# Optimization experiments

Hardware: AMD Instinct MI355X
Metric: run time of the kernel (lower is better)

## Reference

```python
import jax, jax.numpy as jnp
import numpy as np

NEG = -9e15  # sentinel used by the torch module for masked logits


def setup_inputs() -> dict:
    key = jax.random.key(0)
    k_x, k_nl, k_q, k_k, k_v = jax.random.split(key, 5)
    n, m, nhid = 50000, 16, 128
    x = jax.random.normal(k_x, (n, nhid), dtype=jnp.float32)
    neighbor_list = jax.random.randint(k_nl, (n, m), 0, n)  # value n-1 == padding
    # xavier_uniform with gain=1.414 for square (nhid, nhid) matrices
    bound = 1.414 * np.sqrt(6.0 / (nhid + nhid))
    Q = jax.random.uniform(k_q, (nhid, nhid), jnp.float32, -bound, bound)
    K = jax.random.uniform(k_k, (nhid, nhid), jnp.float32, -bound, bound)
    V = jax.random.uniform(k_v, (nhid, nhid), jnp.float32, -bound, bound)
    return {"x": x, "neighbor_list": neighbor_list, "Q": Q, "K": K, "V": V}


def _forward(x, neighbor_list, Q, K, V):
    n, nhid = x.shape
    scare = jnp.asarray(nhid ** 0.5, x.dtype)
    # masks: neighbor index n-1 means padding
    mask = (neighbor_list != n - 1).astype(x.dtype)            # (n, m)
    mask1 = mask[:, :, None] * mask[:, None, :]                # (n, m, m)
    mask2 = jnp.concatenate([jnp.ones((n, 1), x.dtype), mask], axis=1)[:, None, :]  # (n,1,m+1)

    # ---- stage 1: neighbor-level attention ----
    nm = x[neighbor_list]                                      # (n, m, h) gather
    Qn = jnp.einsum('nmk,kh->nmh', nm, Q)
    Kn = jnp.einsum('nmk,kh->nmh', nm, K)
    Vn = jnp.einsum('nmk,kh->nmh', nm, V)
    s = jnp.einsum('nih,njh->nij', Qn, Kn)                     # (n, m, m)
    s = jax.nn.leaky_relu(s, 0.01)
    s = jnp.where(mask1 > 0, s, NEG) * scare                   # faithful: scale after mask
    a = jax.nn.softmax(s, axis=2)                              # dropout is identity (eval)
    nres = jnp.einsum('nij,njh->nih', a, Vn)                   # (n, m, h)

    # ---- stage 2: node-level attention over [self, neighbors] ----
    xr = x[:, None, :]                                         # (n, 1, h)
    cat = jnp.concatenate([xr, nres], axis=1)                  # (n, m+1, h)
    Qx = jnp.einsum('nik,kh->nih', xr, Q)                      # (n, 1, h)
    Kc = jnp.einsum('njk,kh->njh', cat, K)
    Vc = jnp.einsum('njk,kh->njh', cat, V)
    s2 = jnp.einsum('nih,njh->nij', Qx, Kc) * scare            # (n, 1, m+1)
    s2 = jax.nn.leaky_relu(s2, 0.01)
    s2 = jnp.where(mask2 > 0, s2, NEG)
    a2 = jax.nn.softmax(s2, axis=2)
    out = jnp.einsum('nij,njh->nih', a2, Vc)[:, 0, :]          # (n, h)

    # F.normalize: L2 along dim 1, eps 1e-12
    norm = jnp.linalg.norm(out, axis=1, keepdims=True)
    return out / jnp.maximum(norm, 1e-12)


def reference(x, neighbor_list, Q, K, V):
    return _forward(x, neighbor_list, Q, K, V)
```

## Files before the change

### kernel.cpp

```cpp
#include <hip/hip_runtime.h>
#include <math.h>

#define NEG_CONST (-9000000000000000.0f)
#define SCARE 11.313708498984761f

#define DPP_XOR1  0xB1
#define DPP_XOR2  0x4E
#define DPP_XOR7  0x141
#define DPP_XOR15 0x140

template<int CTRL>
__device__ __forceinline__ float dpp_add(float x) {
    int yi = __builtin_amdgcn_update_dpp(0, __float_as_int(x), CTRL, 0xF, 0xF, true);
    return x + __int_as_float(yi);
}
template<int CTRL>
__device__ __forceinline__ float dpp_max(float x) {
    int yi = __builtin_amdgcn_update_dpp(0, __float_as_int(x), CTRL, 0xF, 0xF, true);
    return fmaxf(x, __int_as_float(yi));
}

__device__ __forceinline__ void wave_lds_fence() {
    __builtin_amdgcn_wave_barrier();
    asm volatile("s_waitcnt lgkmcnt(0)" ::: "memory");
    __builtin_amdgcn_wave_barrier();
}

__global__ __launch_bounds__(256) void small_mm_a(const float* __restrict__ Q,
                                                  const float* __restrict__ K,
                                                  const float* __restrict__ V,
                                                  float* __restrict__ QKt,
                                                  float* __restrict__ VV) {
    int r  = blockIdx.x * 8 + (threadIdx.x >> 5);
    int c0 = (threadIdx.x & 31) * 4;
    float a0 = 0.f, a1 = 0.f, a2 = 0.f, a3 = 0.f;
    if (blockIdx.y == 0) {
        for (int k = 0; k < 128; k += 4) {
            float4 q  = *reinterpret_cast<const float4*>(&Q[r * 128 + k]);
            float4 k0 = *reinterpret_cast<const float4*>(&K[(c0 + 0) * 128 + k]);
            float4 k1 = *reinterpret_cast<const float4*>(&K[(c0 + 1) * 128 + k]);
            float4 k2 = *reinterpret_cast<const float4*>(&K[(c0 + 2) * 128 + k]);
            float4 k3 = *reinterpret_cast<const float4*>(&K[(c0 + 3) * 128 + k]);
            a0 += q.x*k0.x + q.y*k0.y + q.z*k0.z + q.w*k0.w;
            a1 += q.x*k1.x + q.y*k1.y + q.z*k1.z + q.w*k1.w;
            a2 += q.x*k2.x + q.y*k2.y + q.z*k2.z + q.w*k2.w;
            a3 += q.x*k3.x + q.y*k3.y + q.z*k3.z + q.w*k3.w;
        }
        float4 o = {a0, a1, a2, a3};
        *reinterpret_cast<float4*>(&QKt[r * 128 + c0]) = o;
    } else {
        for (int k = 0; k < 128; ++k) {
            float a = V[r * 128 + k];
            float4 b = *reinterpret_cast<const float4*>(&V[k * 128 + c0]);
            a0 += a * b.x; a1 += a * b.y; a2 += a * b.z; a3 += a * b.w;
        }
        float4 o = {a0, a1, a2, a3};
        *reinterpret_cast<float4*>(&VV[r * 128 + c0]) = o;
    }
}

__global__ __launch_bounds__(256) void small_mm_b(const float* __restrict__ QKt,
                                                  const float* __restrict__ V,
                                                  float* __restrict__ MT) {
    int r  = blockIdx.x * 8 + (threadIdx.x >> 5);
    int c0 = (threadIdx.x & 31) * 4;
    float a0 = 0.f, a1 = 0.f, a2 = 0.f, a3 = 0.f;
    for (int k = 0; k < 128; k += 4) {
        float4 q  = *reinterpret_cast<const float4*>(&QKt[r * 128 + k]);
        float4 k0 = *reinterpret_cast<const float4*>(&V[(c0 + 0) * 128 + k]);
        float4 k1 = *reinterpret_cast<const float4*>(&V[(c0 + 1) * 128 + k]);
        float4 k2 = *reinterpret_cast<const float4*>(&V[(c0 + 2) * 128 + k]);
        float4 k3 = *reinterpret_cast<const float4*>(&V[(c0 + 3) * 128 + k]);
        a0 += q.x*k0.x + q.y*k0.y + q.z*k0.z + q.w*k0.w;
        a1 += q.x*k1.x + q.y*k1.y + q.z*k1.z + q.w*k1.w;
        a2 += q.x*k2.x + q.y*k2.y + q.z*k2.z + q.w*k2.w;
        a3 += q.x*k3.x + q.y*k3.y + q.z*k3.z + q.w*k3.w;
    }
    float4 o = {a0, a1, a2, a3};
    *reinterpret_cast<float4*>(&MT[r * 128 + c0]) = o;
}

__global__ __launch_bounds__(256) void proj_gemm(
    const float* __restrict__ x,
    const float* __restrict__ W0, const float* __restrict__ W1,
    const float* __restrict__ W2, const float* __restrict__ W3,
    float* __restrict__ O0, float* __restrict__ O1,
    float* __restrict__ O2, float* __restrict__ O3, int n)
{
    __shared__ __align__(16) float xs[32][132];
    __shared__ __align__(16) float ws[32][132];

    const float* Wsel[4] = {W0, W1, W2, W3};
    float*       Osel[4] = {O0, O1, O2, O3};
    const float* W = Wsel[blockIdx.y];
    float*       O = Osel[blockIdx.y];
    int row0 = blockIdx.x * 128;
    int tid = threadIdx.x;
    int tr = tid >> 4, tc = tid & 15;

    float acc[8][8] = {};
    for (int kk = 0; kk < 128; kk += 32) {
        #pragma unroll
        for (int it = 0; it < 4; ++it) {
            int id = tid + it * 256;
            int r = id >> 3;
            int f = id & 7;
            int grow = row0 + r;
            float4 v = (grow < n)
                ? *reinterpret_cast<const float4*>(&x[(size_t)grow * 128 + kk + f * 4])
                : make_float4(0.f, 0.f, 0.f, 0.f);
            xs[f * 4 + 0][r] = v.x; xs[f * 4 + 1][r] = v.y;
            xs[f * 4 + 2][r] = v.z; xs[f * 4 + 3][r] = v.w;
        }
        #pragma unroll
        for (int it = 0; it < 4; ++it) {
            int id = tid + it * 256;
            int k = id >> 5;
            int c4 = id & 31;
            *reinterpret_cast<float4*>(&ws[k][c4 * 4]) =
                *reinterpret_cast<const float4*>(&W[(size_t)(kk + k) * 128 + c4 * 4]);
        }
        __syncthreads();
        #pragma unroll 4
        for (int k = 0; k < 32; ++k) {
            float4 a0 = *reinterpret_cast<const float4*>(&xs[k][tr * 8]);
            float4 a1 = *reinterpret_cast<const float4*>(&xs[k][tr * 8 + 4]);
            float4 b0 = *reinterpret_cast<const float4*>(&ws[k][tc * 8]);
            float4 b1 = *reinterpret_cast<const float4*>(&ws[k][tc * 8 + 4]);
            float av[8] = {a0.x, a0.y, a0.z, a0.w, a1.x, a1.y, a1.z, a1.w};
            float bv[8] = {b0.x, b0.y, b0.z, b0.w, b1.x, b1.y, b1.z, b1.w};
            #pragma unroll
            for (int i2 = 0; i2 < 8; ++i2)
                #pragma unroll
                for (int j2 = 0; j2 < 8; ++j2)
                    acc[i2][j2] += av[i2] * bv[j2];
        }
        __syncthreads();
    }
    #pragma unroll
    for (int i2 = 0; i2 < 8; ++i2) {
        int grow = row0 + tr * 8 + i2;
        if (grow < n) {
            float4 o0 = {acc[i2][0], acc[i2][1], acc[i2][2], acc[i2][3]};
            float4 o1 = {acc[i2][4], acc[i2][5], acc[i2][6], acc[i2][7]};
            *reinterpret_cast<float4*>(&O[(size_t)grow * 128 + tc * 8])     = o0;
            *reinterpret_cast<float4*>(&O[(size_t)grow * 128 + tc * 8 + 4]) = o1;
        }
    }
}

__global__ __launch_bounds__(256, 4) void node_attn(
    const int* __restrict__ nlist,
    const float* __restrict__ x,
    const float* __restrict__ xQK,
    const float* __restrict__ u,
    const float* __restrict__ xV,
    const float* __restrict__ xVV,
    float* __restrict__ outp, int n)
{
    __shared__ __align__(16) float Bs[4][16][132];
    __shared__ __align__(16) int   NLs[4][16];
    __shared__ __align__(16) float Ts[4][16];

    int tid = threadIdx.x;
    int wid = tid >> 6;
    int l   = tid & 63;
    int g   = l >> 2;
    int jj  = l & 3;
    int i = blockIdx.x * 4 + wid;
    if (i >= n) return;

    int nlv = 0;
    if (l < 16) {
        nlv = nlist[(size_t)i * 16 + l];
        NLs[wid][l] = nlv;
    }
    unsigned long long mb = __ballot(l < 16 ? (nlv != n - 1) : 0);
    int nl_g = __shfl(nlv, g, 64);

    float4 A[8];
    size_t rowbase = (size_t)nl_g * 128 + jj * 32;
    #pragma unroll
    for (int k4 = 0; k4 < 8; ++k4) {
        int rc = ((k4 + jj * 2) & 7) * 4;
        A[k4] = *reinterpret_cast<const float4*>(&xQK[rowbase + rc]);
    }
    #pragma unroll
    for (int k4 = 0; k4 < 8; ++k4) {
        int rc = ((k4 + jj * 2) & 7) * 4;
        float4 v = *reinterpret_cast<const float4*>(&x[rowbase + rc]);
        *reinterpret_cast<float4*>(&Bs[wid][g][jj * 32 + rc]) = v;
    }

    float2 qa = *reinterpret_cast<const float2*>(&xQK[(size_t)i * 128 + l * 2]);
    float2 xa = *reinterpret_cast<const float2*>(&x[(size_t)i * 128 + l * 2]);
    float s200 = qa.x * xa.x + qa.y * xa.y;
    s200 = dpp_add<DPP_XOR1>(s200);
    s200 = dpp_add<DPP_XOR2>(s200);
    s200 = dpp_add<DPP_XOR7>(s200);
    s200 = dpp_add<DPP_XOR15>(s200);
    s200 += __shfl_xor(s200, 16, 64);
    s200 += __shfl_xor(s200, 32, 64);

    wave_lds_fence();

    float a[16];
    {
        float sc[16];
        #pragma unroll
        for (int c = 0; c < 16; ++c) {
            float acc = 0.f;
            #pragma unroll
            for (int k4 = 0; k4 < 8; ++k4) {
                int rc = ((k4 + jj * 2) & 7) * 4;
                float4 b = *reinterpret_cast<const float4*>(&Bs[wid][c][jj * 32 + rc]);
                acc += A[k4].x * b.x + A[k4].y * b.y + A[k4].z * b.z + A[k4].w * b.w;
            }
            acc = dpp_add<DPP_XOR1>(acc);
            acc = dpp_add<DPP_XOR2>(acc);
            sc[c] = acc;
        }
        bool rlive = (mb >> g) & 1ULL;
        float m = -3.0e38f;
        #pragma unroll
        for (int c = 0; c < 16; ++c) {
            float s = sc[c];
            float slr = s > 0.f ? s : 0.01f * s;
            bool live = rlive && ((mb >> c) & 1ULL);
            float sm = (live ? slr : NEG_CONST) * SCARE;
            sc[c] = sm;
            m = fmaxf(m, sm);
        }
        float ssum = 0.f;
        #pragma unroll
        for (int c = 0; c < 16; ++c) { float p = __expf(sc[c] - m); a[c] = p; ssum += p; }
        float rs = 1.f / ssum;
        #pragma unroll
        for (int c = 0; c < 16; ++c) a[c] *= rs;
    }

    int nlarr[16];
    {
        int4 nlq[4];
        #pragma unroll
        for (int q4 = 0; q4 < 4; ++q4)
            nlq[q4] = *reinterpret_cast<const int4*>(&NLs[wid][q4 * 4]);
        #pragma unroll
        for (int q4 = 0; q4 < 4; ++q4) {
            nlarr[q4 * 4 + 0] = nlq[q4].x; nlarr[q4 * 4 + 1] = nlq[q4].y;
            nlarr[q4 * 4 + 2] = nlq[q4].z; nlarr[q4 * 4 + 3] = nlq[q4].w;
        }
    }
    float2 vvreg[16];
    #pragma unroll
    for (int k = 0; k < 16; ++k)
        vvreg[k] = *reinterpret_cast<const float2*>(&xVV[(size_t)nlarr[k] * 128 + l * 2]);

    {
        float acc = 0.f;
        #pragma unroll
        for (int k4 = 0; k4 < 8; ++k4) {
            int rc = ((k4 + jj * 2) & 7) * 4;
            float4 uu = *reinterpret_cast<const float4*>(&u[(size_t)i * 128 + jj * 32 + rc]);
            float4 b  = *reinterpret_cast<const float4*>(&Bs[wid][g][jj * 32 + rc]);
            acc += uu.x * b.x + uu.y * b.y + uu.z * b.z + uu.w * b.w;
        }
        acc = dpp_add<DPP_XOR1>(acc);
        acc = dpp_add<DPP_XOR2>(acc);
        if (jj == 0) Ts[wid][g] = acc;
    }
    wave_lds_fence();
    float tarr[16];
    {
        #pragma unroll
        for (int q4 = 0; q4 < 4; ++q4) {
            float4 t4 = *reinterpret_cast<const float4*>(&Ts[wid][q4 * 4]);
            tarr[q4 * 4 + 0] = t4.x; tarr[q4 * 4 + 1] = t4.y;
            tarr[q4 * 4 + 2] = t4.z; tarr[q4 * 4 + 3] = t4.w;
        }
    }

    float lg = 0.f;
    #pragma unroll
    for (int k = 0; k < 16; ++k) lg += a[k] * tarr[k];
    {
        float v = lg * SCARE;
        v = v > 0.f ? v : 0.01f * v;
        lg = ((mb >> g) & 1ULL) ? v : NEG_CONST;
    }
    float v0 = s200 * SCARE;
    v0 = v0 > 0.f ? v0 : 0.01f * v0;

    float m17 = lg;
    m17 = dpp_max<DPP_XOR7>(m17);
    m17 = dpp_max<DPP_XOR15>(m17);
    m17 = fmaxf(m17, __shfl_xor(m17, 16, 64));
    m17 = fmaxf(m17, __shfl_xor(m17, 32, 64));
    m17 = fmaxf(m17, v0);
    float pg = __expf(lg - m17);
    float sg = pg;
    sg = dpp_add<DPP_XOR7>(sg);
    sg = dpp_add<DPP_XOR15>(sg);
    sg += __shfl_xor(sg, 16, 64);
    sg += __shfl_xor(sg, 32, 64);
    float p0 = __expf(v0 - m17);
    float inv = 1.f / (sg + p0);
    float a2g = pg * inv;
    float a20 = p0 * inv;

    float w[16];
    #pragma unroll
    for (int k = 0; k < 16; ++k) {
        float wv = a2g * a[k];
        wv = dpp_add<DPP_XOR7>(wv);
        wv = dpp_add<DPP_XOR15>(wv);
        wv += __shfl_xor(wv, 16, 64);
        wv += __shfl_xor(wv, 32, 64);
        w[k] = wv;
    }

    float2 xv = *reinterpret_cast<const float2*>(&xV[(size_t)i * 128 + l * 2]);
    float o0 = a20 * xv.x, o1 = a20 * xv.y;
    #pragma unroll
    for (int k = 0; k < 16; ++k) {
        o0 += w[k] * vvreg[k].x;
        o1 += w[k] * vvreg[k].y;
    }
    float sq = o0 * o0 + o1 * o1;
    sq = dpp_add<DPP_XOR1>(sq);
    sq = dpp_add<DPP_XOR2>(sq);
    sq = dpp_add<DPP_XOR7>(sq);
    sq = dpp_add<DPP_XOR15>(sq);
    sq += __shfl_xor(sq, 16, 64);
    sq += __shfl_xor(sq, 32, 64);
    float d = fmaxf(sqrtf(sq), 1e-12f);
    float rd = 1.f / d;
    float2 o = {o0 * rd, o1 * rd};
    *reinterpret_cast<float2*>(&outp[(size_t)i * 128 + l * 2]) = o;
}

extern "C" void kernel_launch(void* const* d_in, const int* in_sizes, int n_in,
                              void* d_out, int out_size, void* d_ws, size_t ws_size,
                              hipStream_t stream) {
    const float* x     = (const float*)d_in[0];
    const int*   nlist = (const int*)d_in[1];
    const float* Q     = (const float*)d_in[2];
    const float* K     = (const float*)d_in[3];
    const float* V     = (const float*)d_in[4];
    float* out = (float*)d_out;
    int n = in_sizes[0] / 128;

    float* ws   = (float*)d_ws;
    float* QKt  = ws;
    float* MT   = ws + 16384;
    float* VV   = ws + 32768;
    float* xQK  = ws + 49152;
    size_t stride = (size_t)n * 128;
    float* uarr = xQK + stride;
    float* xV   = uarr + stride;
    float* xVV  = xV + stride;

    small_mm_a<<<dim3(16, 2), 256, 0, stream>>>(Q, K, V, QKt, VV);
    small_mm_b<<<dim3(16), 256, 0, stream>>>(QKt, V, MT);
    dim3 g2((n + 127) / 128, 4);
    proj_gemm<<<g2, 256, 0, stream>>>(x, QKt, MT, V, VV, xQK, uarr, xV, xVV, n);
    node_attn<<<(n + 3) / 4, 256, 0, stream>>>(nlist, x, xQK, uarr, xV, xVV, out, n);
}
```

Baseline: 316.4 us.

## Use direct global-to-LDS loads for neighbor rows with one wave per node

The node_attn kernel now runs one 64-thread wave per node instead of four waves per block. The gathered neighbor x rows go straight to LDS through global_load_lds, with a permuted layout so the score loop reads are conflict-free. This is meant to remove the register round trip for the staging copy and to let the xQK loads overlap with the async LDS fill. In exchange there are many more small blocks, and the code depends on the exact byte layout the LDS-direct loads produce.

```diff
diff --git a/kernel.cpp b/kernel.cpp
--- a/kernel.cpp
+++ b/kernel.cpp
@@ -23,6 +23,11 @@
 __device__ __forceinline__ void wave_lds_fence() {
     __builtin_amdgcn_wave_barrier();
     asm volatile("s_waitcnt lgkmcnt(0)" ::: "memory");
+    __builtin_amdgcn_wave_barrier();
+}
+__device__ __forceinline__ void wave_vm_fence() {
+    __builtin_amdgcn_wave_barrier();
+    asm volatile("s_waitcnt vmcnt(0) lgkmcnt(0)" ::: "memory");
     __builtin_amdgcn_wave_barrier();
 }
 
@@ -149,7 +154,7 @@
     }
 }
 
-__global__ __launch_bounds__(256, 4) void node_attn(
+__global__ __launch_bounds__(64, 5) void node_attn(
     const int* __restrict__ nlist,
     const float* __restrict__ x,
     const float* __restrict__ xQK,
@@ -158,38 +163,35 @@
     const float* __restrict__ xVV,
     float* __restrict__ outp, int n)
 {
-    __shared__ __align__(16) float Bs[4][16][132];
-    __shared__ __align__(16) int   NLs[4][16];
-    __shared__ __align__(16) float Ts[4][16];
-
-    int tid = threadIdx.x;
-    int wid = tid >> 6;
-    int l   = tid & 63;
-    int g   = l >> 2;
-    int jj  = l & 3;
-    int i = blockIdx.x * 4 + wid;
-    if (i >= n) return;
+    __shared__ __align__(16) float Bs[2048];
+    __shared__ __align__(16) int   NLs[16];
+    __shared__ __align__(16) float Ts[16];
+
+    const int l  = threadIdx.x;
+    const int g  = l >> 2;
+    const int jj = l & 3;
+    const int i  = blockIdx.x;
 
     int nlv = 0;
     if (l < 16) {
         nlv = nlist[(size_t)i * 16 + l];
-        NLs[wid][l] = nlv;
+        NLs[l] = nlv;
     }
     unsigned long long mb = __ballot(l < 16 ? (nlv != n - 1) : 0);
-    int nl_g = __shfl(nlv, g, 64);
-
-    float4 A[8];
-    size_t rowbase = (size_t)nl_g * 128 + jj * 32;
-    #pragma unroll
-    for (int k4 = 0; k4 < 8; ++k4) {
-        int rc = ((k4 + jj * 2) & 7) * 4;
-        A[k4] = *reinterpret_cast<const float4*>(&xQK[rowbase + rc]);
-    }
-    #pragma unroll
-    for (int k4 = 0; k4 < 8; ++k4) {
-        int rc = ((k4 + jj * 2) & 7) * 4;
-        float4 v = *reinterpret_cast<const float4*>(&x[rowbase + rc]);
-        *reinterpret_cast<float4*>(&Bs[wid][g][jj * 32 + rc]) = v;
+
+    {
+        int sub   = l & 31;
+        int sigma = ((sub & 3) << 3) | (sub >> 2);
+        int half  = l >> 5;
+        #pragma unroll
+        for (int p = 0; p < 8; ++p) {
+            int nr = __shfl(nlv, 2 * p + half, 64);
+            const float* src = &x[(size_t)nr * 128 + sigma * 4];
+            __builtin_amdgcn_global_load_lds(
+                (const __attribute__((address_space(1))) unsigned int*)src,
+                (__attribute__((address_space(3))) unsigned int*)&Bs[p * 256],
+                16, 0, 0);
+        }
     }
 
     float2 qa = *reinterpret_cast<const float2*>(&xQK[(size_t)i * 128 + l * 2]);
@@ -202,18 +204,27 @@
     s200 += __shfl_xor(s200, 16, 64);
     s200 += __shfl_xor(s200, 32, 64);
 
-    wave_lds_fence();
+    int nl_g = __shfl(nlv, g, 64);
+    float4 A[8];
+    {
+        const float* ab = &xQK[(size_t)nl_g * 128 + jj * 32];
+        #pragma unroll
+        for (int k4 = 0; k4 < 8; ++k4)
+            A[k4] = *reinterpret_cast<const float4*>(&ab[k4 * 4]);
+    }
+
+    wave_vm_fence();
 
     float a[16];
     {
         float sc[16];
         #pragma unroll
         for (int c = 0; c < 16; ++c) {
+            const float* bb = &Bs[c * 128 + jj * 4];
             float acc = 0.f;
             #pragma unroll
             for (int k4 = 0; k4 < 8; ++k4) {
-                int rc = ((k4 + jj * 2) & 7) * 4;
-                float4 b = *reinterpret_cast<const float4*>(&Bs[wid][c][jj * 32 + rc]);
+                float4 b = *reinterpret_cast<const float4*>(&bb[k4 * 16]);
                 acc += A[k4].x * b.x + A[k4].y * b.y + A[k4].z * b.z + A[k4].w * b.w;
             }
             acc = dpp_add<DPP_XOR1>(acc);
@@ -244,7 +255,7 @@
         int4 nlq[4];
         #pragma unroll
         for (int q4 = 0; q4 < 4; ++q4)
-            nlq[q4] = *reinterpret_cast<const int4*>(&NLs[wid][q4 * 4]);
+            nlq[q4] = *reinterpret_cast<const int4*>(&NLs[q4 * 4]);
         #pragma unroll
         for (int q4 = 0; q4 < 4; ++q4) {
             nlarr[q4 * 4 + 0] = nlq[q4].x; nlarr[q4 * 4 + 1] = nlq[q4].y;
@@ -260,21 +271,21 @@
         float acc = 0.f;
         #pragma unroll
         for (int k4 = 0; k4 < 8; ++k4) {
-            int rc = ((k4 + jj * 2) & 7) * 4;
-            float4 uu = *reinterpret_cast<const float4*>(&u[(size_t)i * 128 + jj * 32 + rc]);
-            float4 b  = *reinterpret_cast<const float4*>(&Bs[wid][g][jj * 32 + rc]);
+            int kx = (k4 + g) & 7;
+            float4 b  = *reinterpret_cast<const float4*>(&Bs[g * 128 + kx * 16 + jj * 4]);
+            float4 uu = *reinterpret_cast<const float4*>(&u[(size_t)i * 128 + jj * 32 + kx * 4]);
             acc += uu.x * b.x + uu.y * b.y + uu.z * b.z + uu.w * b.w;
         }
         acc = dpp_add<DPP_XOR1>(acc);
         acc = dpp_add<DPP_XOR2>(acc);
-        if (jj == 0) Ts[wid][g] = acc;
+        if (jj == 0) Ts[g] = acc;
     }
     wave_lds_fence();
     float tarr[16];
     {
         #pragma unroll
         for (int q4 = 0; q4 < 4; ++q4) {
-            float4 t4 = *reinterpret_cast<const float4*>(&Ts[wid][q4 * 4]);
+            float4 t4 = *reinterpret_cast<const float4*>(&Ts[q4 * 4]);
             tarr[q4 * 4 + 0] = t4.x; tarr[q4 * 4 + 1] = t4.y;
             tarr[q4 * 4 + 2] = t4.z; tarr[q4 * 4 + 3] = t4.w;
         }
@@ -364,5 +375,5 @@
     small_mm_b<<<dim3(16), 256, 0, stream>>>(QKt, V, MT);
     dim3 g2((n + 127) / 128, 4);
     proj_gemm<<<g2, 256, 0, stream>>>(x, QKt, MT, V, VV, xQK, uarr, xV, xVV, n);
-    node_attn<<<(n + 3) / 4, 256, 0, stream>>>(nlist, x, xQK, uarr, xV, xVV, out, n);
-}
+    node_attn<<<n, 64, 0, stream>>>(nlist, x, xQK, uarr, xV, xVV, out, n);
+}
```

Result: no change. 319.3 us (+0.9%).
